# Kernel tuning notes

Hardware: AMD Instinct MI355X
Metric: run time of the kernel (lower is better)

The kernel has to match this reference:

```python
import jax, jax.numpy as jnp
import numpy as np

DIM = 256; WS = 8; HEADS = 8; HD = DIM // HEADS; SCALE = HD ** -0.5; MLP_HIDDEN = 1024
B = 8; H = 128; W = 128


def setup_inputs() -> dict:
    key = jax.random.key(0)
    ks = jax.random.split(key, 16)
    def nrm(k, shape, s=0.02):
        return jax.random.normal(k, shape, jnp.float32) * s
    # relative position index (same construction as torch buffer)
    coords = np.stack(np.meshgrid(np.arange(WS), np.arange(WS), indexing='ij')).reshape(2, -1)
    rel = (coords[:, :, None] - coords[:, None, :]).transpose(1, 2, 0).astype(np.int64)
    rel[..., 0] += WS - 1; rel[..., 1] += WS - 1; rel[..., 0] *= 2 * WS - 1
    rel_idx = jnp.asarray(rel.sum(-1), jnp.int32)  # (64,64) in [0,225)
    return dict(
        x=nrm(ks[0], (B, H, W, DIM), 1.0),
        rel_table=nrm(ks[1], ((2 * WS - 1) ** 2, HEADS)),
        qkv_w=nrm(ks[2], (3 * DIM, DIM)), qkv_b=nrm(ks[3], (3 * DIM,)),
        qkv2_w=nrm(ks[4], (3 * DIM, DIM)), qkv2_b=nrm(ks[5], (3 * DIM,)),
        proj_ln_w=jnp.ones((DIM,), jnp.float32), proj_ln_b=jnp.zeros((DIM,), jnp.float32),
        proj_w=nrm(ks[6], (DIM, DIM)), proj_b=nrm(ks[7], (DIM,)),
        proj2_ln_w=jnp.ones((DIM,), jnp.float32), proj2_ln_b=jnp.zeros((DIM,), jnp.float32),
        proj2_w=nrm(ks[8], (DIM, DIM)), proj2_b=nrm(ks[9], (DIM,)),
        norm1_w=jnp.ones((DIM,), jnp.float32), norm1_b=jnp.zeros((DIM,), jnp.float32),
        norm2_w=jnp.ones((DIM,), jnp.float32), norm2_b=jnp.zeros((DIM,), jnp.float32),
        fc1_w=nrm(ks[10], (MLP_HIDDEN, DIM)), fc1_b=nrm(ks[11], (MLP_HIDDEN,)),
        fc2_w=nrm(ks[12], (DIM, MLP_HIDDEN)), fc2_b=nrm(ks[13], (DIM,)),
        rel_idx=rel_idx,
    )


def _ln(x, w, b):
    mu = x.mean(-1, keepdims=True)
    var = ((x - mu) ** 2).mean(-1, keepdims=True)
    return (x - mu) / jnp.sqrt(var + 1e-5) * w + b


def _mha(tokens, wqkv, bqkv, bias=None):
    Bt, N, C = tokens.shape
    qkv = (tokens @ wqkv.T + bqkv).reshape(Bt, N, 3, HEADS, HD).transpose(2, 0, 3, 1, 4)
    q, k, v = qkv[0] * SCALE, qkv[1], qkv[2]
    attn = jnp.einsum('bhnd,bhmd->bhnm', q, k)
    if bias is not None:
        attn = attn + bias  # (1,heads,N,N) relative position bias
    attn = jax.nn.softmax(attn, axis=-1)
    out = jnp.einsum('bhnm,bhmd->bhnd', attn, v)
    return out.transpose(0, 2, 1, 3).reshape(Bt, N, C)


def _pos_sine(h, w, c):
    # PositionEmbeddingSine(normalize=True), mask all-zero -> cumsum = 1..h / 1..w
    npf = c // 2
    scale = 2.0 * np.pi; eps = 1e-5
    y = jnp.arange(1, h + 1, dtype=jnp.float32); y = y / (y[-1] + eps) * scale
    xw = jnp.arange(1, w + 1, dtype=jnp.float32); xw = xw / (xw[-1] + eps) * scale
    dim_t = 10000.0 ** ((2.0 * (jnp.arange(npf) // 2)) / npf)
    def enc(e):  # (L,) -> (L,npf) interleaved sin/cos
        p = e[:, None] / dim_t
        return jnp.stack([jnp.sin(p[:, 0::2]), jnp.cos(p[:, 1::2])], axis=-1).reshape(e.shape[0], npf)
    py = enc(y); px = enc(xw)
    return jnp.concatenate([jnp.broadcast_to(py[:, None, :], (h, w, npf)),
                            jnp.broadcast_to(px[None, :, :], (h, w, npf))], axis=-1)  # (h,w,c)


def _upsample_ac(x, oh, ow):
    # bilinear, align_corners=True; x: (B,h,w,C)
    Bn, h, w, C = x.shape
    def idx(n, o):
        s = jnp.linspace(0.0, n - 1.0, o)
        i0 = jnp.floor(s).astype(jnp.int32)
        i1 = jnp.minimum(i0 + 1, n - 1)
        return i0, i1, s - i0
    y0, y1, ty = idx(h, oh)
    x = x[:, y0] * (1 - ty)[None, :, None, None] + x[:, y1] * ty[None, :, None, None]
    x0, x1, tx = idx(w, ow)
    x = x[:, :, x0] * (1 - tx)[None, None, :, None] + x[:, :, x1] * tx[None, None, :, None]
    return x


def reference(x, rel_table, qkv_w, qkv_b, qkv2_w, qkv2_b,
              proj_ln_w, proj_ln_b, proj_w, proj_b,
              proj2_ln_w, proj2_ln_b, proj2_w, proj2_b,
              norm1_w, norm1_b, norm2_w, norm2_b,
              fc1_w, fc1_b, fc2_w, fc2_b, rel_idx):
    Bn, Hh, Ww, C = x.shape  # H,W divisible by WS -> padding is a no-op
    nh, nw = Hh // WS, Ww // WS
    N = WS * WS
    shortcut = x
    # window partition -> (B*nh*nw, N, C)
    xw = x.reshape(Bn, nh, WS, nw, WS, C).transpose(0, 1, 3, 2, 4, 5).reshape(-1, N, C)
    bias = rel_table[rel_idx.reshape(-1)].reshape(N, N, HEADS).transpose(2, 0, 1)[None]
    xw = _mha(xw, qkv_w, qkv_b, bias)
    xw = xw.reshape(Bn, nh, nw, WS, WS, C).transpose(0, 1, 3, 2, 4, 5).reshape(Bn, Hh, Ww, C)
    x = shortcut + xw
    x = x + (_ln(x, proj_ln_w, proj_ln_b) @ proj_w.T + proj_b)
    shortcut = x
    # global branch: avgpool each window, sine pos enc, full attention, bilinear upsample
    xg = x.reshape(Bn, nh, WS, nw, WS, C).mean(axis=(2, 4))  # (B,nh,nw,C)
    xg = xg + _pos_sine(nh, nw, C)[None]
    xg = _mha(xg.reshape(Bn, nh * nw, C), qkv2_w, qkv2_b).reshape(Bn, nh, nw, C)
    xg = _upsample_ac(xg, Hh, Ww)
    x = shortcut + xg
    x = x + (_ln(x, proj2_ln_w, proj2_ln_b) @ proj2_w.T + proj2_b)
    h = _ln(x, norm1_w, norm1_b)
    h = jax.nn.gelu(h @ fc1_w.T + fc1_b, approximate=False) @ fc2_w.T + fc2_b
    x = x + h
    return _ln(x, norm2_w, norm2_b)
```

## Files before the change

### kernel.cpp

```cpp
#include <hip/hip_runtime.h>
#include <math.h>

#define DEV __device__ __forceinline__

constexpr int NTOK = 131072;
constexpr int TOKS_PER_B = 16384;
constexpr float SCALE_F = 0.17677669529663687f;

typedef float f32x4 __attribute__((ext_vector_type(4)));
typedef _Float16 half8 __attribute__((ext_vector_type(8)));
typedef _Float16 half2v __attribute__((ext_vector_type(2)));
typedef unsigned short us8 __attribute__((ext_vector_type(8)));

#if defined(__has_builtin)
#if __has_builtin(__builtin_amdgcn_fdot2)
#define HAS_FDOT2 1
#endif
#endif

DEV float gelu1(float v) { return 0.5f * v * (1.f + erff(v * 0.7071067811865476f)); }
DEV unsigned short f2h(float x) { _Float16 h = (_Float16)x; return __builtin_bit_cast(unsigned short, h); }
DEV float h2f(unsigned short u) { return (float)__builtin_bit_cast(_Float16, u); }

DEV float dot2acc(unsigned qp, unsigned kp, float acc) {
#ifdef HAS_FDOT2
  return __builtin_amdgcn_fdot2(__builtin_bit_cast(half2v, qp),
                                __builtin_bit_cast(half2v, kp), acc, false);
#else
  return acc + h2f((unsigned short)(qp & 0xffff)) * h2f((unsigned short)(kp & 0xffff))
             + h2f((unsigned short)(qp >> 16)) * h2f((unsigned short)(kp >> 16));
#endif
}

__global__ void cvtw16_k(const float* __restrict__ w, unsigned short* __restrict__ dst, int n) {
  const int i = (blockIdx.x * 256 + threadIdx.x) * 4;
  float4 v = *(const float4*)(w + i);
  ushort4 h, l;
  h.x = f2h(v.x); l.x = f2h(v.x - h2f(h.x));
  h.y = f2h(v.y); l.y = f2h(v.y - h2f(h.y));
  h.z = f2h(v.z); l.z = f2h(v.z - h2f(h.z));
  h.w = f2h(v.w); l.w = f2h(v.w - h2f(h.w));
  *(ushort4*)(dst + i) = h;
  *(ushort4*)(dst + n + i) = l;
}

__global__ void biasprep_k(const float* __restrict__ rel_table, const int* __restrict__ rel_idx,
                           float* __restrict__ biasT) {
  const int i = blockIdx.x * 256 + threadIdx.x;
  const int h = i >> 12, mr = i & 4095, m = mr >> 6, r = mr & 63;
  biasT[i] = rel_table[rel_idx[r * 64 + m] * 8 + h];
}

template <int AMODE, bool RES, bool GELU, bool OUTH, bool STATS, bool FINLN>
__launch_bounds__(256)
__global__ void gemm16(const void* __restrict__ Ain, const unsigned short* __restrict__ Wp,
                       const float* __restrict__ bias, void* __restrict__ outv,
                       const float* __restrict__ stats,
                       const float* __restrict__ lnw, const float* __restrict__ lnb,
                       float* __restrict__ statsOut,
                       const float* __restrict__ fw, const float* __restrict__ fb,
                       int M, int N, int K) {
  __shared__ unsigned short As[64][40];
  __shared__ unsigned short Wh[256][40], Wl[256][40];
  const int t = threadIdx.x;
  const int lane = t & 63, wid = t >> 6;
  const int m0 = blockIdx.x * 64, n0 = blockIdx.y * 256;
  const unsigned short* Wlp = Wp + (size_t)N * K;

  f32x4 acc[4][4];
#pragma unroll
  for (int i = 0; i < 4; ++i)
#pragma unroll
    for (int j = 0; j < 4; ++j) acc[i][j] = (f32x4){0.f, 0.f, 0.f, 0.f};

  const int fr = lane & 15, ko = (lane >> 4) * 8;
  const int ar = t >> 2, ac = (t & 3) * 8;
  float mu = 0.f, rs = 1.f;
  if (AMODE == 1) {
    mu = stats[(size_t)(m0 + ar) * 2];
    rs = stats[(size_t)(m0 + ar) * 2 + 1];
  }

  for (int k0 = 0; k0 < K; k0 += 32) {
    if (AMODE == 2) {
      *(us8*)&As[ar][ac] =
          *(const us8*)((const unsigned short*)Ain + (size_t)(m0 + ar) * K + k0 + ac);
    } else {
      const float* Af = (const float*)Ain;
      float4 v0 = *(const float4*)(Af + (size_t)(m0 + ar) * K + k0 + ac);
      float4 v1 = *(const float4*)(Af + (size_t)(m0 + ar) * K + k0 + ac + 4);
      if (AMODE == 1) {
        float4 w0 = *(const float4*)(lnw + k0 + ac), w1 = *(const float4*)(lnw + k0 + ac + 4);
        float4 b0 = *(const float4*)(lnb + k0 + ac), b1 = *(const float4*)(lnb + k0 + ac + 4);
        v0.x = (v0.x - mu) * rs * w0.x + b0.x;  v0.y = (v0.y - mu) * rs * w0.y + b0.y;
        v0.z = (v0.z - mu) * rs * w0.z + b0.z;  v0.w = (v0.w - mu) * rs * w0.w + b0.w;
        v1.x = (v1.x - mu) * rs * w1.x + b1.x;  v1.y = (v1.y - mu) * rs * w1.y + b1.y;
        v1.z = (v1.z - mu) * rs * w1.z + b1.z;  v1.w = (v1.w - mu) * rs * w1.w + b1.w;
      }
      us8 hh;
      hh[0] = f2h(v0.x); hh[1] = f2h(v0.y); hh[2] = f2h(v0.z); hh[3] = f2h(v0.w);
      hh[4] = f2h(v1.x); hh[5] = f2h(v1.y); hh[6] = f2h(v1.z); hh[7] = f2h(v1.w);
      *(us8*)&As[ar][ac] = hh;
    }
#pragma unroll
    for (int it = 0; it < 4; ++it) {
      const int id = t + it * 256;
      const int rn = id >> 2, kc = (id & 3) * 8;
      const size_t g = (size_t)(n0 + rn) * K + k0 + kc;
      *(us8*)&Wh[rn][kc] = *(const us8*)(Wp + g);
      *(us8*)&Wl[rn][kc] = *(const us8*)(Wlp + g);
    }
    __syncthreads();
    half8 a4[4], bh4[4], bl4[4];
#pragma unroll
    for (int i = 0; i < 4; ++i) {
      a4[i] = __builtin_bit_cast(half8, *(const us8*)&As[i * 16 + fr][ko]);
      bh4[i] = __builtin_bit_cast(half8, *(const us8*)&Wh[wid * 64 + i * 16 + fr][ko]);
      bl4[i] = __builtin_bit_cast(half8, *(const us8*)&Wl[wid * 64 + i * 16 + fr][ko]);
    }
#pragma unroll
    for (int i = 0; i < 4; ++i)
#pragma unroll
      for (int j = 0; j < 4; ++j) {
        acc[i][j] = __builtin_amdgcn_mfma_f32_16x16x32_f16(a4[i], bh4[j], acc[i][j], 0, 0, 0);
        acc[i][j] = __builtin_amdgcn_mfma_f32_16x16x32_f16(a4[i], bl4[j], acc[i][j], 0, 0, 0);
      }
    __syncthreads();
  }
  const int g4 = (lane >> 4) * 4;
#pragma unroll
  for (int i = 0; i < 4; ++i)
#pragma unroll
    for (int j = 0; j < 4; ++j) {
      const int col = n0 + wid * 64 + j * 16 + fr;
      const float bb = bias[col];
#pragma unroll
      for (int r4 = 0; r4 < 4; ++r4) {
        const int row = m0 + i * 16 + g4 + r4;
        float v = acc[i][j][r4] + bb;
        if (GELU) v = gelu1(v);
        if (RES) v += ((const float*)outv)[(size_t)row * N + col];
        acc[i][j][r4] = v;
      }
    }
  if (STATS || FINLN) {
    __shared__ float rsum[4][64], rsq[4][64];
    float ps[4][4], pq[4][4];
#pragma unroll
    for (int i = 0; i < 4; ++i)
#pragma unroll
      for (int r4 = 0; r4 < 4; ++r4) {
        float s = acc[i][0][r4] + acc[i][1][r4] + acc[i][2][r4] + acc[i][3][r4];
        float q = acc[i][0][r4] * acc[i][0][r4] + acc[i][1][r4] * acc[i][1][r4] +
                  acc[i][2][r4] * acc[i][2][r4] + acc[i][3][r4] * acc[i][3][r4];
        ps[i][r4] = s; pq[i][r4] = q;
      }
#pragma unroll
    for (int off = 1; off < 16; off <<= 1)
#pragma unroll
      for (int i = 0; i < 4; ++i)
#pragma unroll
        for (int r4 = 0; r4 < 4; ++r4) {
          ps[i][r4] += __shfl_xor(ps[i][r4], off, 64);
          pq[i][r4] += __shfl_xor(pq[i][r4], off, 64);
        }
    if (fr == 0) {
#pragma unroll
      for (int i = 0; i < 4; ++i)
#pragma unroll
        for (int r4 = 0; r4 < 4; ++r4) {
          rsum[wid][i * 16 + g4 + r4] = ps[i][r4];
          rsq[wid][i * 16 + g4 + r4] = pq[i][r4];
        }
    }
    __syncthreads();
#pragma unroll
    for (int i = 0; i < 4; ++i)
#pragma unroll
      for (int r4 = 0; r4 < 4; ++r4) {
        const int rl = i * 16 + g4 + r4;
        const float S = rsum[0][rl] + rsum[1][rl] + rsum[2][rl] + rsum[3][rl];
        const float Q = rsq[0][rl] + rsq[1][rl] + rsq[2][rl] + rsq[3][rl];
        const float mu2 = S * (1.f / 256.f);
        const float var = Q * (1.f / 256.f) - mu2 * mu2;
        const float rstd = 1.f / sqrtf(var + 1e-5f);
        if (STATS && wid == 0 && fr == 0) {
          statsOut[(size_t)(m0 + rl) * 2] = mu2;
          statsOut[(size_t)(m0 + rl) * 2 + 1] = rstd;
        }
        if (FINLN) {
#pragma unroll
          for (int j = 0; j < 4; ++j) {
            const int col = n0 + wid * 64 + j * 16 + fr;
            acc[i][j][r4] = (acc[i][j][r4] - mu2) * rstd * fw[col] + fb[col];
          }
        }
      }
  }
#pragma unroll
  for (int i = 0; i < 4; ++i)
#pragma unroll
    for (int j = 0; j < 4; ++j) {
      const int col = n0 + wid * 64 + j * 16 + fr;
#pragma unroll
      for (int r4 = 0; r4 < 4; ++r4) {
        const int row = m0 + i * 16 + g4 + r4;
        if (OUTH) ((unsigned short*)outv)[(size_t)row * N + col] = f2h(acc[i][j][r4]);
        else ((float*)outv)[(size_t)row * N + col] = acc[i][j][r4];
      }
    }
}

__launch_bounds__(64)
__global__ void winattn_k(const unsigned short* __restrict__ qkv, const float* __restrict__ xin,
                          float* __restrict__ X, const float* __restrict__ biasT, int b0) {
  __shared__ unsigned short klds[64][40];
  __shared__ float vlds[64][36];
  const int p = blockIdx.x;
  const int brel = p >> 11, rest = p & 2047;
  const int widx = rest >> 3, h = rest & 7;
  const int wy = widx >> 4, wx = widx & 15;
  const int r = threadIdx.x;
  const int tl = (wy * 8 + (r >> 3)) * 128 + wx * 8 + (r & 7);
  const unsigned short* qr = qkv + ((size_t)brel * TOKS_PER_B + tl) * 768 + h * 32;
  uint4 qa = __builtin_bit_cast(uint4, *(const us8*)(qr + 0));
  uint4 qb = __builtin_bit_cast(uint4, *(const us8*)(qr + 8));
  uint4 qc = __builtin_bit_cast(uint4, *(const us8*)(qr + 16));
  uint4 qd = __builtin_bit_cast(uint4, *(const us8*)(qr + 24));
#pragma unroll
  for (int jj = 0; jj < 4; ++jj)
    *(us8*)&klds[r][jj * 8] = *(const us8*)(qr + 256 + jj * 8);
#pragma unroll
  for (int jj = 0; jj < 4; ++jj) {
    us8 vv = *(const us8*)(qr + 512 + jj * 8);
    float4 f0, f1;
    f0.x = h2f(vv[0]); f0.y = h2f(vv[1]); f0.z = h2f(vv[2]); f0.w = h2f(vv[3]);
    f1.x = h2f(vv[4]); f1.y = h2f(vv[5]); f1.z = h2f(vv[6]); f1.w = h2f(vv[7]);
    *(float4*)&vlds[r][jj * 8] = f0;
    *(float4*)&vlds[r][jj * 8 + 4] = f1;
  }
  __syncthreads();

  const float* bf = biasT + h * 4096;
  float o[32];
#pragma unroll
  for (int e = 0; e < 32; ++e) o[e] = 0.f;
  float l = 0.f;
#pragma unroll 4
  for (int m = 0; m < 64; ++m) {
    uint4 k0 = *(const uint4*)&klds[m][0];
    uint4 k1 = *(const uint4*)&klds[m][8];
    uint4 k2 = *(const uint4*)&klds[m][16];
    uint4 k3 = *(const uint4*)&klds[m][24];
    float s = 0.f;
    s = dot2acc(qa.x, k0.x, s); s = dot2acc(qa.y, k0.y, s);
    s = dot2acc(qa.z, k0.z, s); s = dot2acc(qa.w, k0.w, s);
    s = dot2acc(qb.x, k1.x, s); s = dot2acc(qb.y, k1.y, s);
    s = dot2acc(qb.z, k1.z, s); s = dot2acc(qb.w, k1.w, s);
    s = dot2acc(qc.x, k2.x, s); s = dot2acc(qc.y, k2.y, s);
    s = dot2acc(qc.z, k2.z, s); s = dot2acc(qc.w, k2.w, s);
    s = dot2acc(qd.x, k3.x, s); s = dot2acc(qd.y, k3.y, s);
    s = dot2acc(qd.z, k3.z, s); s = dot2acc(qd.w, k3.w, s);
    const float pm = __expf(s * SCALE_F + bf[m * 64 + r]);
    l += pm;
    const float* vr = vlds[m];
#pragma unroll
    for (int e4 = 0; e4 < 8; ++e4) {
      float4 v4 = *(const float4*)(vr + e4 * 4);
      o[e4 * 4 + 0] += pm * v4.x; o[e4 * 4 + 1] += pm * v4.y;
      o[e4 * 4 + 2] += pm * v4.z; o[e4 * 4 + 3] += pm * v4.w;
    }
  }
  const float inv = 1.f / l;
  const size_t go = (size_t)((b0 + brel) * TOKS_PER_B + tl) * 256 + h * 32;
#pragma unroll
  for (int j4 = 0; j4 < 8; ++j4) {
    float4 xi = *(const float4*)(xin + go + j4 * 4);
    float4 rr;
    rr.x = o[j4*4+0] * inv + xi.x; rr.y = o[j4*4+1] * inv + xi.y;
    rr.z = o[j4*4+2] * inv + xi.z; rr.w = o[j4*4+3] * inv + xi.w;
    *(float4*)(X + go + j4 * 4) = rr;
  }
}

__global__ void lnstats_k(const float* __restrict__ X, float* __restrict__ stats) {
  const int lane = threadIdx.x & 63;
  const int wave = threadIdx.x >> 6;
  for (int tok = blockIdx.x * 4 + wave; tok < NTOK; tok += gridDim.x * 4) {
    float4 v = *(const float4*)(X + (size_t)tok * 256 + lane * 4);
    float s = v.x + v.y + v.z + v.w;
    float q = v.x*v.x + v.y*v.y + v.z*v.z + v.w*v.w;
#pragma unroll
    for (int off = 32; off > 0; off >>= 1) {
      s += __shfl_xor(s, off, 64);
      q += __shfl_xor(q, off, 64);
    }
    if (lane == 0) {
      const float m = s * (1.f / 256.f);
      const float var = q * (1.f / 256.f) - m * m;
      stats[(size_t)tok * 2] = m;
      stats[(size_t)tok * 2 + 1] = 1.f / sqrtf(var + 1e-5f);
    }
  }
}

__global__ void poolsine_k(const float* __restrict__ X, float* __restrict__ G0) {
  const int c = threadIdx.x;
  const int wx = blockIdx.x & 15, wy = (blockIdx.x >> 4) & 15, b = blockIdx.x >> 8;
  const float* base = X + ((size_t)(b * 128 + wy * 8) * 128 + wx * 8) * 256 + c;
  float s = 0.f;
  for (int ry = 0; ry < 8; ++ry)
#pragma unroll
    for (int rx = 0; rx < 8; ++rx) s += base[((size_t)ry * 128 + rx) * 256];
  s *= (1.f / 64.f);
  const float sc = 6.283185307179586f / (16.f + 1e-5f);
  const int cc = c & 127;
  const float d = powf(10000.f, (float)(cc >> 1) * (1.f / 64.f));
  const float e = ((c < 128 ? (float)(wy + 1) : (float)(wx + 1)) * sc) / d;
  const float pos = (cc & 1) ? cosf(e) : sinf(e);
  G0[(size_t)blockIdx.x * 256 + c] = s + pos;
}

__global__ void gattn_k(const float* __restrict__ G1, float* __restrict__ G2) {
  const int b = blockIdx.x, h = blockIdx.y, n = threadIdx.x;
  const float* qp = G1 + ((size_t)b * 256 + n) * 768 + h * 32;
  float q[32];
#pragma unroll
  for (int j4 = 0; j4 < 8; ++j4) {
    float4 v = *(const float4*)(qp + j4 * 4);
    q[j4*4+0] = v.x * SCALE_F; q[j4*4+1] = v.y * SCALE_F;
    q[j4*4+2] = v.z * SCALE_F; q[j4*4+3] = v.w * SCALE_F;
  }
  const float* kb = G1 + (size_t)b * 256 * 768 + 256 + h * 32;
  const float* vb = kb + 256;
  float out[32];
#pragma unroll
  for (int j = 0; j < 32; ++j) out[j] = 0.f;
  float mx = -3.4e38f, l = 0.f;
  for (int m = 0; m < 256; ++m) {
    const float* kr = kb + (size_t)m * 768;
    float s = 0.f;
#pragma unroll
    for (int j4 = 0; j4 < 8; ++j4) {
      float4 k4 = *(const float4*)(kr + j4 * 4);
      s += q[j4*4+0]*k4.x + q[j4*4+1]*k4.y + q[j4*4+2]*k4.z + q[j4*4+3]*k4.w;
    }
    const float mn = fmaxf(mx, s);
    const float corr = __expf(mx - mn);
    const float p = __expf(s - mn);
    l = l * corr + p;
    const float* vr = vb + (size_t)m * 768;
#pragma unroll
    for (int j4 = 0; j4 < 8; ++j4) {
      float4 v4 = *(const float4*)(vr + j4 * 4);
      out[j4*4+0] = out[j4*4+0]*corr + p*v4.x; out[j4*4+1] = out[j4*4+1]*corr + p*v4.y;
      out[j4*4+2] = out[j4*4+2]*corr + p*v4.z; out[j4*4+3] = out[j4*4+3]*corr + p*v4.w;
    }
    mx = mn;
  }
  const float inv = 1.f / l;
  float* op = G2 + ((size_t)b * 256 + n) * 256 + h * 32;
#pragma unroll
  for (int j4 = 0; j4 < 8; ++j4) {
    float4 r;
    r.x = out[j4*4+0]*inv; r.y = out[j4*4+1]*inv;
    r.z = out[j4*4+2]*inv; r.w = out[j4*4+3]*inv;
    *(float4*)(op + j4 * 4) = r;
  }
}

__global__ void upadd_k(float* __restrict__ X, const float* __restrict__ G2,
                        float* __restrict__ stats) {
  const int c = threadIdx.x;
  const int tok = blockIdx.x;
  const int j = tok & 127, i = (tok >> 7) & 127, b = tok >> 14;
  const float sy = i * (15.f / 127.f);
  const float sx = j * (15.f / 127.f);
  const int y0 = (int)sy; const float ty = sy - y0; const int y1 = min(y0 + 1, 15);
  const int x0 = (int)sx; const float tx = sx - x0; const int x1 = min(x0 + 1, 15);
  const float* gb = G2 + (size_t)b * 256 * 256;
  const float v00 = gb[((size_t)(y0 * 16 + x0)) * 256 + c];
  const float v01 = gb[((size_t)(y0 * 16 + x1)) * 256 + c];
  const float v10 = gb[((size_t)(y1 * 16 + x0)) * 256 + c];
  const float v11 = gb[((size_t)(y1 * 16 + x1)) * 256 + c];
  const float vy0 = v00 * (1.f - ty) + v10 * ty;
  const float vy1 = v01 * (1.f - ty) + v11 * ty;
  const float val = X[(size_t)tok * 256 + c] + vy0 * (1.f - tx) + vy1 * tx;
  X[(size_t)tok * 256 + c] = val;
  float s = val, q = val * val;
#pragma unroll
  for (int off = 32; off > 0; off >>= 1) {
    s += __shfl_xor(s, off, 64);
    q += __shfl_xor(q, off, 64);
  }
  __shared__ float red[8];
  const int lane = c & 63, wave = c >> 6;
  if (lane == 0) { red[wave * 2] = s; red[wave * 2 + 1] = q; }
  __syncthreads();
  if (c == 0) {
    const float S = red[0] + red[2] + red[4] + red[6];
    const float Q = red[1] + red[3] + red[5] + red[7];
    const float m = S * (1.f / 256.f);
    const float var = Q * (1.f / 256.f) - m * m;
    stats[(size_t)tok * 2] = m;
    stats[(size_t)tok * 2 + 1] = 1.f / sqrtf(var + 1e-5f);
  }
}

extern "C" void kernel_launch(void* const* d_in, const int* in_sizes, int n_in,
                              void* d_out, int out_size, void* d_ws, size_t ws_size,
                              hipStream_t stream) {
  const float* x          = (const float*)d_in[0];
  const float* rel_table  = (const float*)d_in[1];
  const float* qkv_w      = (const float*)d_in[2];
  const float* qkv_b      = (const float*)d_in[3];
  const float* qkv2_w     = (const float*)d_in[4];
  const float* qkv2_b     = (const float*)d_in[5];
  const float* proj_ln_w  = (const float*)d_in[6];
  const float* proj_ln_b  = (const float*)d_in[7];
  const float* proj_w     = (const float*)d_in[8];
  const float* proj_b     = (const float*)d_in[9];
  const float* proj2_ln_w = (const float*)d_in[10];
  const float* proj2_ln_b = (const float*)d_in[11];
  const float* proj2_w    = (const float*)d_in[12];
  const float* proj2_b    = (const float*)d_in[13];
  const float* norm1_w    = (const float*)d_in[14];
  const float* norm1_b    = (const float*)d_in[15];
  const float* norm2_w    = (const float*)d_in[16];
  const float* norm2_b    = (const float*)d_in[17];
  const float* fc1_w      = (const float*)d_in[18];
  const float* fc1_b      = (const float*)d_in[19];
  const float* fc2_w      = (const float*)d_in[20];
  const float* fc2_b      = (const float*)d_in[21];
  const int*   rel_idx    = (const int*)d_in[22];

  float* X = (float*)d_out;
  char* wsb = (char*)d_ws;
  float* stats = (float*)wsb;
  float* G0 = (float*)(wsb + (size_t)1048576);
  float* G1 = G0 + (size_t)2048 * 256;
  float* G2 = G1 + (size_t)2048 * 768;
  unsigned short* WCVT = (unsigned short*)(G2 + (size_t)2048 * 256);
  float* BIASF = (float*)((char*)WCVT + (size_t)4194304);
  char* BIG = (char*)BIASF + 131072;
  unsigned short* BIGH = (unsigned short*)BIG;
  const size_t fixed = (size_t)(BIG - wsb);
  const size_t avail = ws_size > fixed ? ws_size - fixed : 0;

  unsigned short* w_qkv  = WCVT;
  unsigned short* w_qkv2 = WCVT + 393216;
  unsigned short* w_proj = WCVT + 786432;
  unsigned short* w_proj2= WCVT + 917504;
  unsigned short* w_fc1  = WCVT + 1048576;
  unsigned short* w_fc2  = WCVT + 1572864;
  cvtw16_k<<<192, 256, 0, stream>>>(qkv_w,   w_qkv,   196608);
  cvtw16_k<<<192, 256, 0, stream>>>(qkv2_w,  w_qkv2,  196608);
  cvtw16_k<<<64,  256, 0, stream>>>(proj_w,  w_proj,   65536);
  cvtw16_k<<<64,  256, 0, stream>>>(proj2_w, w_proj2,  65536);
  cvtw16_k<<<256, 256, 0, stream>>>(fc1_w,   w_fc1,   262144);
  cvtw16_k<<<256, 256, 0, stream>>>(fc2_w,   w_fc2,   262144);
  biasprep_k<<<128, 256, 0, stream>>>(rel_table, rel_idx, BIASF);

  int st = 16384;
  if (avail >= (size_t)268435456) st = 131072;
  else if (avail >= (size_t)134217728) st = 65536;
  else if (avail >= (size_t)67108864) st = 32768;
  const bool one_shot = avail >= (size_t)NTOK * 768 * 2;

  if (one_shot) {
    gemm16<0, false, false, true, false, false><<<dim3(NTOK / 64, 3), 256, 0, stream>>>(
        x, w_qkv, qkv_b, BIGH, nullptr, nullptr, nullptr, nullptr, nullptr, nullptr,
        NTOK, 768, 256);
    winattn_k<<<16384, 64, 0, stream>>>(BIGH, x, X, BIASF, 0);
  } else {
    for (int b = 0; b < 8; ++b) {
      gemm16<0, false, false, true, false, false><<<dim3(TOKS_PER_B / 64, 3), 256, 0, stream>>>(
          x + (size_t)b * TOKS_PER_B * 256, w_qkv, qkv_b, BIGH,
          nullptr, nullptr, nullptr, nullptr, nullptr, nullptr, TOKS_PER_B, 768, 256);
      winattn_k<<<2048, 64, 0, stream>>>(BIGH, x, X, BIASF, b);
    }
  }
  lnstats_k<<<1024, 256, 0, stream>>>(X, stats);
  gemm16<1, true, false, false, false, false><<<dim3(NTOK / 64, 1), 256, 0, stream>>>(
      X, w_proj, proj_b, X, stats, proj_ln_w, proj_ln_b, nullptr, nullptr, nullptr,
      NTOK, 256, 256);
  poolsine_k<<<2048, 256, 0, stream>>>(X, G0);
  gemm16<0, false, false, false, false, false><<<dim3(32, 3), 256, 0, stream>>>(
      G0, w_qkv2, qkv2_b, G1, nullptr, nullptr, nullptr, nullptr, nullptr, nullptr,
      2048, 768, 256);
  gattn_k<<<dim3(8, 8), 256, 0, stream>>>(G1, G2);
  upadd_k<<<NTOK, 256, 0, stream>>>(X, G2, stats);
  gemm16<1, true, false, false, true, false><<<dim3(NTOK / 64, 1), 256, 0, stream>>>(
      X, w_proj2, proj2_b, X, stats, proj2_ln_w, proj2_ln_b, stats, nullptr, nullptr,
      NTOK, 256, 256);
  for (int s0 = 0; s0 < NTOK; s0 += st) {
    gemm16<1, false, true, true, false, false><<<dim3(st / 64, 4), 256, 0, stream>>>(
        X + (size_t)s0 * 256, w_fc1, fc1_b, BIGH, stats + (size_t)s0 * 2,
        norm1_w, norm1_b, nullptr, nullptr, nullptr, st, 1024, 256);
    gemm16<2, true, false, false, false, true><<<dim3(st / 64, 1), 256, 0, stream>>>(
        BIGH, w_fc2, fc2_b, X + (size_t)s0 * 256, nullptr, nullptr, nullptr, nullptr,
        norm2_w, norm2_b, st, 256, 1024);
  }
}
```

Before: 1.790 ms.

## Load GEMM tiles directly to LDS with swizzled layout and swap grid axes

```diff
diff --git a/kernel.cpp b/kernel.cpp
--- a/kernel.cpp
+++ b/kernel.cpp
@@ -31,6 +31,16 @@
              + h2f((unsigned short)(qp >> 16)) * h2f((unsigned short)(kp >> 16));
 #endif
 }
+
+DEV int swz_row(int p) { return ((p >> 2) & ~1) | (((p >> 2) ^ (p >> 4)) & 1); }
+DEV int swz_gran(int p) {
+  return ((p ^ (p >> 2) ^ (p >> 4)) & 1) | ((((p >> 1) ^ (p >> 3)) & 1) << 1);
+}
+
+#define GLOAD16(src, dst)                                                        \
+  __builtin_amdgcn_global_load_lds(                                              \
+      (const __attribute__((address_space(1))) void*)(src),                      \
+      (__attribute__((address_space(3))) void*)(dst), 16, 0, 0)
 
 __global__ void cvtw16_k(const float* __restrict__ w, unsigned short* __restrict__ dst, int n) {
   const int i = (blockIdx.x * 256 + threadIdx.x) * 4;
@@ -60,11 +70,11 @@
                        float* __restrict__ statsOut,
                        const float* __restrict__ fw, const float* __restrict__ fb,
                        int M, int N, int K) {
-  __shared__ unsigned short As[64][40];
-  __shared__ unsigned short Wh[256][40], Wl[256][40];
+  __shared__ __align__(16) char Asm[64 * 64];
+  __shared__ __align__(16) char Wsm[2 * 256 * 64];
   const int t = threadIdx.x;
   const int lane = t & 63, wid = t >> 6;
-  const int m0 = blockIdx.x * 64, n0 = blockIdx.y * 256;
+  const int m0 = blockIdx.y * 64, n0 = blockIdx.x * 256;
   const unsigned short* Wlp = Wp + (size_t)N * K;
 
   f32x4 acc[4][4];
@@ -73,50 +83,67 @@
 #pragma unroll
     for (int j = 0; j < 4; ++j) acc[i][j] = (f32x4){0.f, 0.f, 0.f, 0.f};
 
-  const int fr = lane & 15, ko = (lane >> 4) * 8;
-  const int ar = t >> 2, ac = (t & 3) * 8;
-  float mu = 0.f, rs = 1.f;
-  if (AMODE == 1) {
-    mu = stats[(size_t)(m0 + ar) * 2];
-    rs = stats[(size_t)(m0 + ar) * 2 + 1];
+  const int fr = lane & 15, G = lane >> 4;
+  const int sw16 = (((4 * fr + G) ^ (fr & 7)) << 4);
+
+  const float* Afrow = nullptr;
+  const unsigned short* Ahrow = nullptr;
+  int aG = 0;
+  float mu = 0.f, rsg = 1.f;
+  if constexpr (AMODE == 2) {
+    const int p = wid * 64 + lane;
+    Ahrow = (const unsigned short*)Ain + (size_t)(m0 + swz_row(p)) * K + swz_gran(p) * 8;
+  } else {
+    const int p = t;
+    const int aR = swz_row(p);
+    aG = swz_gran(p);
+    Afrow = (const float*)Ain + (size_t)(m0 + aR) * K + aG * 8;
+    if constexpr (AMODE == 1) {
+      mu = stats[(size_t)(m0 + aR) * 2];
+      rsg = stats[(size_t)(m0 + aR) * 2 + 1];
+    }
+  }
+  const unsigned short* wsrc[8];
+  int wdst[8];
+#pragma unroll
+  for (int j = 0; j < 8; ++j) {
+    const int plane = j >> 2;
+    const int bs = (wid * 4 + (j & 3)) * 64;
+    const int p = bs + lane;
+    wsrc[j] = (plane ? Wlp : Wp) + (size_t)(n0 + swz_row(p)) * K + swz_gran(p) * 8;
+    wdst[j] = plane * (256 * 64) + bs * 16;
   }
 
   for (int k0 = 0; k0 < K; k0 += 32) {
-    if (AMODE == 2) {
-      *(us8*)&As[ar][ac] =
-          *(const us8*)((const unsigned short*)Ain + (size_t)(m0 + ar) * K + k0 + ac);
+#pragma unroll
+    for (int j = 0; j < 8; ++j) GLOAD16(wsrc[j] + k0, Wsm + wdst[j]);
+    if constexpr (AMODE == 2) {
+      GLOAD16(Ahrow + k0, Asm + wid * 1024);
     } else {
-      const float* Af = (const float*)Ain;
-      float4 v0 = *(const float4*)(Af + (size_t)(m0 + ar) * K + k0 + ac);
-      float4 v1 = *(const float4*)(Af + (size_t)(m0 + ar) * K + k0 + ac + 4);
-      if (AMODE == 1) {
-        float4 w0 = *(const float4*)(lnw + k0 + ac), w1 = *(const float4*)(lnw + k0 + ac + 4);
-        float4 b0 = *(const float4*)(lnb + k0 + ac), b1 = *(const float4*)(lnb + k0 + ac + 4);
-        v0.x = (v0.x - mu) * rs * w0.x + b0.x;  v0.y = (v0.y - mu) * rs * w0.y + b0.y;
-        v0.z = (v0.z - mu) * rs * w0.z + b0.z;  v0.w = (v0.w - mu) * rs * w0.w + b0.w;
-        v1.x = (v1.x - mu) * rs * w1.x + b1.x;  v1.y = (v1.y - mu) * rs * w1.y + b1.y;
-        v1.z = (v1.z - mu) * rs * w1.z + b1.z;  v1.w = (v1.w - mu) * rs * w1.w + b1.w;
+      float4 v0 = *(const float4*)(Afrow + k0);
+      float4 v1 = *(const float4*)(Afrow + k0 + 4);
+      if constexpr (AMODE == 1) {
+        const int kc = k0 + aG * 8;
+        float4 w0 = *(const float4*)(lnw + kc), w1 = *(const float4*)(lnw + kc + 4);
+        float4 b0 = *(const float4*)(lnb + kc), b1 = *(const float4*)(lnb + kc + 4);
+        v0.x = (v0.x - mu) * rsg * w0.x + b0.x;  v0.y = (v0.y - mu) * rsg * w0.y + b0.y;
+        v0.z = (v0.z - mu) * rsg * w0.z + b0.z;  v0.w = (v0.w - mu) * rsg * w0.w + b0.w;
+        v1.x = (v1.x - mu) * rsg * w1.x + b1.x;  v1.y = (v1.y - mu) * rsg * w1.y + b1.y;
+        v1.z = (v1.z - mu) * rsg * w1.z + b1.z;  v1.w = (v1.w - mu) * rsg * w1.w + b1.w;
       }
       us8 hh;
       hh[0] = f2h(v0.x); hh[1] = f2h(v0.y); hh[2] = f2h(v0.z); hh[3] = f2h(v0.w);
       hh[4] = f2h(v1.x); hh[5] = f2h(v1.y); hh[6] = f2h(v1.z); hh[7] = f2h(v1.w);
-      *(us8*)&As[ar][ac] = hh;
-    }
-#pragma unroll
-    for (int it = 0; it < 4; ++it) {
-      const int id = t + it * 256;
-      const int rn = id >> 2, kc = (id & 3) * 8;
-      const size_t g = (size_t)(n0 + rn) * K + k0 + kc;
-      *(us8*)&Wh[rn][kc] = *(const us8*)(Wp + g);
-      *(us8*)&Wl[rn][kc] = *(const us8*)(Wlp + g);
+      *(us8*)(Asm + t * 16) = hh;
     }
     __syncthreads();
     half8 a4[4], bh4[4], bl4[4];
 #pragma unroll
     for (int i = 0; i < 4; ++i) {
-      a4[i] = __builtin_bit_cast(half8, *(const us8*)&As[i * 16 + fr][ko]);
-      bh4[i] = __builtin_bit_cast(half8, *(const us8*)&Wh[wid * 64 + i * 16 + fr][ko]);
-      bl4[i] = __builtin_bit_cast(half8, *(const us8*)&Wl[wid * 64 + i * 16 + fr][ko]);
+      a4[i] = __builtin_bit_cast(half8, *(const us8*)(Asm + i * 1024 + sw16));
+      bh4[i] = __builtin_bit_cast(half8, *(const us8*)(Wsm + wid * 4096 + i * 1024 + sw16));
+      bl4[i] = __builtin_bit_cast(half8,
+               *(const us8*)(Wsm + 256 * 64 + wid * 4096 + i * 1024 + sw16));
     }
 #pragma unroll
     for (int i = 0; i < 4; ++i)
@@ -150,10 +177,9 @@
     for (int i = 0; i < 4; ++i)
 #pragma unroll
       for (int r4 = 0; r4 < 4; ++r4) {
-        float s = acc[i][0][r4] + acc[i][1][r4] + acc[i][2][r4] + acc[i][3][r4];
-        float q = acc[i][0][r4] * acc[i][0][r4] + acc[i][1][r4] * acc[i][1][r4] +
-                  acc[i][2][r4] * acc[i][2][r4] + acc[i][3][r4] * acc[i][3][r4];
-        ps[i][r4] = s; pq[i][r4] = q;
+        ps[i][r4] = acc[i][0][r4] + acc[i][1][r4] + acc[i][2][r4] + acc[i][3][r4];
+        pq[i][r4] = acc[i][0][r4] * acc[i][0][r4] + acc[i][1][r4] * acc[i][1][r4] +
+                    acc[i][2][r4] * acc[i][2][r4] + acc[i][3][r4] * acc[i][3][r4];
       }
 #pragma unroll
     for (int off = 1; off < 16; off <<= 1)
@@ -468,36 +494,36 @@
   const bool one_shot = avail >= (size_t)NTOK * 768 * 2;
 
   if (one_shot) {
-    gemm16<0, false, false, true, false, false><<<dim3(NTOK / 64, 3), 256, 0, stream>>>(
+    gemm16<0, false, false, true, false, false><<<dim3(3, NTOK / 64), 256, 0, stream>>>(
         x, w_qkv, qkv_b, BIGH, nullptr, nullptr, nullptr, nullptr, nullptr, nullptr,
         NTOK, 768, 256);
     winattn_k<<<16384, 64, 0, stream>>>(BIGH, x, X, BIASF, 0);
   } else {
     for (int b = 0; b < 8; ++b) {
-      gemm16<0, false, false, true, false, false><<<dim3(TOKS_PER_B / 64, 3), 256, 0, stream>>>(
+      gemm16<0, false, false, true, false, false><<<dim3(3, TOKS_PER_B / 64), 256, 0, stream>>>(
           x + (size_t)b * TOKS_PER_B * 256, w_qkv, qkv_b, BIGH,
           nullptr, nullptr, nullptr, nullptr, nullptr, nullptr, TOKS_PER_B, 768, 256);
       winattn_k<<<2048, 64, 0, stream>>>(BIGH, x, X, BIASF, b);
     }
   }
   lnstats_k<<<1024, 256, 0, stream>>>(X, stats);
-  gemm16<1, true, false, false, false, false><<<dim3(NTOK / 64, 1), 256, 0, stream>>>(
+  gemm16<1, true, false, false, false, false><<<dim3(1, NTOK / 64), 256, 0, stream>>>(
       X, w_proj, proj_b, X, stats, proj_ln_w, proj_ln_b, nullptr, nullptr, nullptr,
       NTOK, 256, 256);
   poolsine_k<<<2048, 256, 0, stream>>>(X, G0);
-  gemm16<0, false, false, false, false, false><<<dim3(32, 3), 256, 0, stream>>>(
+  gemm16<0, false, false, false, false, false><<<dim3(3, 32), 256, 0, stream>>>(
       G0, w_qkv2, qkv2_b, G1, nullptr, nullptr, nullptr, nullptr, nullptr, nullptr,
       2048, 768, 256);
   gattn_k<<<dim3(8, 8), 256, 0, stream>>>(G1, G2);
   upadd_k<<<NTOK, 256, 0, stream>>>(X, G2, stats);
-  gemm16<1, true, false, false, true, false><<<dim3(NTOK / 64, 1), 256, 0, stream>>>(
+  gemm16<1, true, false, false, true, false><<<dim3(1, NTOK / 64), 256, 0, stream>>>(
       X, w_proj2, proj2_b, X, stats, proj2_ln_w, proj2_ln_b, stats, nullptr, nullptr,
       NTOK, 256, 256);
   for (int s0 = 0; s0 < NTOK; s0 += st) {
-    gemm16<1, false, true, true, false, false><<<dim3(st / 64, 4), 256, 0, stream>>>(
+    gemm16<1, false, true, true, false, false><<<dim3(4, st / 64), 256, 0, stream>>>(
         X + (size_t)s0 * 256, w_fc1, fc1_b, BIGH, stats + (size_t)s0 * 2,
         norm1_w, norm1_b, nullptr, nullptr, nullptr, st, 1024, 256);
-    gemm16<2, true, false, false, false, true><<<dim3(st / 64, 1), 256, 0, stream>>>(
+    gemm16<2, true, false, false, false, true><<<dim3(1, st / 64), 256, 0, stream>>>(
         BIGH, w_fc2, fc2_b, X + (size_t)s0 * 256, nullptr, nullptr, nullptr, nullptr,
         norm2_w, norm2_b, st, 256, 1024);
   }
```

After: 1.761 ms. Within noise of the previous version (-1.6%).
